# Optimization experiments

Measured on AMD Instinct MI355X. Metric: run time of the kernel, lower is better.

The kernel has to match this reference:

```python
import jax, jax.numpy as jnp
import numpy as np

D_MODEL = 512
D_STATE = 16
D_CONV = 3
EXPAND = 2
D_INNER = EXPAND * D_MODEL          # 1024
DT_RANK = -(-D_MODEL // 16)          # ceil(d_model/16) = 32
BATCH = 2
SEQ = 1024


def setup_inputs() -> dict:
    key = jax.random.key(0)
    ks = jax.random.split(key, 8)
    s = 0.02
    x = jax.random.normal(ks[0], (BATCH, SEQ, D_MODEL), jnp.float32)
    in_proj_w = jax.random.normal(ks[1], (2 * D_INNER, D_MODEL), jnp.float32) * s
    conv_w = jax.random.normal(ks[2], (D_INNER, 1, D_CONV), jnp.float32) * 0.2  # depthwise (out, in/groups=1, K)
    conv_b = jnp.zeros((D_INNER,), jnp.float32)
    x_proj_w = jax.random.normal(ks[3], (DT_RANK + 4 * D_STATE + 1, D_INNER), jnp.float32) * s
    dt_std = DT_RANK ** -0.5
    dt_w = jax.random.uniform(ks[4], (D_INNER, DT_RANK), jnp.float32, -dt_std, dt_std)
    dt = jnp.exp(jax.random.uniform(ks[5], (D_INNER,), jnp.float32)
                 * (np.log(0.1) - np.log(0.001)) + np.log(0.001))
    dt = jnp.maximum(dt, 1e-4)
    dt_b = dt + jnp.log(-jnp.expm1(-dt))  # inverse-softplus init, as in torch code
    A_log = jnp.log(jnp.tile(jnp.arange(1, D_STATE + 1, dtype=jnp.float32)[None, :], (D_INNER, 1)))
    A_imag = np.pi * jax.random.uniform(ks[6], (D_INNER, D_STATE), jnp.float32)
    D_skip = jnp.ones((D_INNER,), jnp.float32)
    out_proj_w = jax.random.normal(ks[7], (D_MODEL, D_INNER), jnp.float32) * s
    return {"x": x, "in_proj_w": in_proj_w, "conv_w": conv_w, "conv_b": conv_b,
            "x_proj_w": x_proj_w, "dt_w": dt_w, "dt_b": dt_b,
            "A_log": A_log, "A_imag": A_imag, "D_skip": D_skip,
            "out_proj_w": out_proj_w}


def _combine(c1, c2):
    # linear recurrence h_t = a_t * h_{t-1} + u_t as an associative op
    a1, u1 = c1
    a2, u2 = c2
    return a1 * a2, a2 * u1 + u2


def reference(x, in_proj_w, conv_w, conv_b, x_proj_w, dt_w, dt_b,
              A_log, A_imag, D_skip, out_proj_w):
    Bsz, L, _ = x.shape
    d_state = A_log.shape[1]
    dt_rank = dt_w.shape[1]

    xz = x @ in_proj_w.T                     # (B, L, 2*D_inner)
    xi, z = jnp.split(xz, 2, axis=-1)

    # causal depthwise conv1d (torch pads both sides K-1 then slices [:L] == left-pad K-1)
    xc = jax.lax.conv_general_dilated(
        xi.transpose(0, 2, 1), conv_w, window_strides=(1,),
        padding=[(D_CONV - 1, 0)], dimension_numbers=("NCH", "OIH", "NCH"),
        feature_group_count=conv_w.shape[0])
    xc = (xc + conv_b[None, :, None]).transpose(0, 2, 1)   # (B, L, D_inner)
    xc = jax.nn.silu(xc)

    A = -jnp.exp(A_log) + 1j * A_imag         # (D_inner, N) complex64

    proj = xc @ x_proj_w.T                     # (B, L, dt_rank + 4N + 1)
    splits = np.cumsum([dt_rank, d_state, d_state, d_state, d_state])
    delta_raw, B_re, B_im, C_re, C_im, lam = jnp.split(proj, splits, axis=-1)
    delta = jax.nn.softplus(delta_raw @ dt_w.T + dt_b)     # (B, L, D_inner)
    lam = jax.nn.sigmoid(lam)                              # (B, L, 1)
    Bc = B_re + 1j * B_im                                  # (B, L, N)
    Cc = C_re + 1j * C_im                                  # (B, L, N)

    # selective_scan_v3 (trapezoidal discretization)
    alpha = jnp.exp(delta[..., None] * A[None, None])      # (B, L, D, N) complex
    Bx = Bc[:, :, None, :] * xc[..., None]                 # (B, L, D, N) complex
    beta = (1.0 - lam)[..., None] * delta[..., None] * alpha
    gamma = lam[..., None] * delta[..., None]
    Bx_prev = jnp.pad(Bx[:, :-1], ((0, 0), (1, 0), (0, 0), (0, 0)))
    u = beta * Bx_prev + gamma * Bx                        # (B, L, D, N) complex

    _, hs = jax.lax.associative_scan(_combine, (alpha, u), axis=1)

    y = jnp.real(jnp.sum(hs * jnp.conj(Cc)[:, :, None, :], axis=-1))  # (B, L, D)
    y = y + D_skip * xc
    out = (y * jax.nn.silu(z)) @ out_proj_w.T              # (B, L, d_model)
    return out
```

## Files before the change

kernel.cpp:

```cpp
#include <hip/hip_runtime.h>

constexpr int B  = 2, L = 1024, DM = 512, DI = 1024, NST = 16, PW = 97;
constexpr int ML = B * L;
constexpr int NCHUNK = 32, CL = L / NCHUNK;
constexpr int NLANES = B * DI * NST;

#define DEV_INLINE __device__ __forceinline__

typedef __attribute__((ext_vector_type(8))) short bf16x8;
typedef __attribute__((ext_vector_type(4))) float f32x4;

DEV_INLINE float sigmoidf_(float x) { return 1.f / (1.f + __expf(-x)); }
DEV_INLINE unsigned short f2bf(float f) {
  unsigned int u = __float_as_uint(f);
  return (unsigned short)((u + 0x7FFFu + ((u >> 16) & 1u)) >> 16);
}

#if __has_builtin(__builtin_amdgcn_exp2f)
#define EXP2F(x) __builtin_amdgcn_exp2f(x)
#else
#define EXP2F(x) exp2f(x)
#endif
#if __has_builtin(__builtin_amdgcn_sinf)
#define SINR(x) __builtin_amdgcn_sinf(x)
#define COSR(x) __builtin_amdgcn_cosf(x)
#else
#define SINR(x) __sinf((x) * 6.2831853f)
#define COSR(x) __cosf((x) * 6.2831853f)
#endif

#if __has_builtin(__builtin_amdgcn_global_load_lds)
#define HAVE_GLDS 1
#define GLOAD16(g, l)                                                         \
  __builtin_amdgcn_global_load_lds(                                           \
      (const __attribute__((address_space(1))) unsigned int*)(g),             \
      (__attribute__((address_space(3))) unsigned int*)(l), 16, 0, 0)
#else
#define HAVE_GLDS 0
#endif

DEV_INLINE void sincos_poly(float th, float& s, float& c) {
  float t2 = th * th;
  float u = fmaf(t2, -1.9841270e-4f, 8.3333333e-3f);
  u = fmaf(t2, u, -0.16666667f);
  u = fmaf(t2, u, 1.f);
  s = th * u;
  float v = fmaf(t2, -1.3888889e-3f, 4.1666667e-2f);
  v = fmaf(t2, v, -0.5f);
  c = fmaf(t2, v, 1.f);
}

template <int CTRL>
DEV_INLINE float dpp_add(float v) {
  int x = __builtin_amdgcn_update_dpp(0, __float_as_int(v), CTRL, 0xF, 0xF, true);
  return v + __int_as_float(x);
}

__global__ __launch_bounds__(256) void cvt4_k(
    const float* __restrict__ i0, unsigned short* __restrict__ o0, int n0,
    const float* __restrict__ i1, unsigned short* __restrict__ o1, int n1,
    const float* __restrict__ i2, unsigned short* __restrict__ o2, int n2,
    const float* __restrict__ xw, unsigned short* __restrict__ xwpb) {
  int i = blockIdx.x * 256 + threadIdx.x;
  if (i < n0) {
    float4 v = ((const float4*)i0)[i];
    ((ushort4*)o0)[i] = make_ushort4(f2bf(v.x), f2bf(v.y), f2bf(v.z), f2bf(v.w));
  } else if (i < n0 + n1) {
    int off = i - n0;
    float4 v = ((const float4*)i1)[off];
    ((ushort4*)o1)[off] = make_ushort4(f2bf(v.x), f2bf(v.y), f2bf(v.z), f2bf(v.w));
  } else if (i < n0 + n1 + n2) {
    int off = i - n0 - n1;
    float4 v = ((const float4*)i2)[off];
    ((ushort4*)o2)[off] = make_ushort4(f2bf(v.x), f2bf(v.y), f2bf(v.z), f2bf(v.w));
  } else {
    int off = i - n0 - n1 - n2;
    if (off < 128 * 256) {
      int row = off >> 8;
      float4 v = (row < PW) ? ((const float4*)xw)[off] : make_float4(0, 0, 0, 0);
      ((ushort4*)xwpb)[off] = make_ushort4(f2bf(v.x), f2bf(v.y), f2bf(v.z), f2bf(v.w));
    }
  }
}

DEV_INLINE int swz(int row, int kb) { return (row << 7) + (kb ^ ((row & 7) << 4)); }

DEV_INLINE void stage16(const short* g, char* l) {
#if HAVE_GLDS
  GLOAD16(g, l);
#else
  *(bf16x8*)l = *(const bf16x8*)g;
#endif
}

#define GEMM_STAGE(Abase, Wbase)                                              \
  _Pragma("unroll")                                                           \
  for (int i = 0; i < 2; ++i) {                                               \
    int off = i * 4096 + tid * 16;                                            \
    int row = off >> 7, kb = off & 127;                                       \
    int kel = (kb ^ ((row & 7) << 4)) >> 1;                                   \
    stage16(Abase + (size_t)(bm + row) * K + k0 + kel, ldsb + off);           \
    stage16(Wbase + (size_t)(bn + row) * K + k0 + kel, ldsb + 8192 + off);    \
  }

#define GEMM_MFMA_BODY                                                        \
  _Pragma("unroll")                                                           \
  for (int ks = 0; ks < 2; ++ks) {                                            \
    const int kb = ks * 64 + ((lane >> 4) << 4);                              \
    bf16x8 af = *(const bf16x8*)(ldsb + swz(wv * 16 + (lane & 15), kb));      \
    _Pragma("unroll")                                                         \
    for (int nb = 0; nb < 4; ++nb) {                                          \
      bf16x8 bfv = *(const bf16x8*)(ldsb + 8192 + swz(nb * 16 + (lane & 15), kb)); \
      acc[nb] = __builtin_amdgcn_mfma_f32_16x16x32_bf16(af, bfv, acc[nb], 0, 0, 0); \
    }                                                                         \
  }

__global__ __launch_bounds__(256) void gemm_bf16_64(
    const short* __restrict__ A, const short* __restrict__ W,
    float* __restrict__ C, int M, int N, int K) {
  __shared__ char ldsb[16384];
  const int tid = threadIdx.x;
  const int lane = tid & 63, wv = tid >> 6;
  const int bm = blockIdx.y * 64, bn = blockIdx.x * 64;

  f32x4 acc[4];
#pragma unroll
  for (int nb = 0; nb < 4; ++nb) acc[nb] = (f32x4){0.f, 0.f, 0.f, 0.f};

  for (int k0 = 0; k0 < K; k0 += 64) {
    GEMM_STAGE(A, W)
    __syncthreads();
    GEMM_MFMA_BODY
    __syncthreads();
  }
#pragma unroll
  for (int nb = 0; nb < 4; ++nb) {
    int col = bn + nb * 16 + (lane & 15);
    int row0 = bm + wv * 16 + ((lane >> 4) << 2);
#pragma unroll
    for (int j = 0; j < 4; ++j)
      C[(size_t)(row0 + j) * N + col] = acc[nb][j];
  }
}

__global__ __launch_bounds__(256) void gemm_bf16_sk(
    const short* __restrict__ A, const short* __restrict__ W,
    float* __restrict__ P, int M, int N, int K, int KS) {
  __shared__ char ldsb[16384];
  const int tid = threadIdx.x;
  const int lane = tid & 63, wv = tid >> 6;
  const int bm = blockIdx.y * 64, bn = blockIdx.x * 64;
  const int kz = blockIdx.z * KS;
  float* Cp = P + (size_t)blockIdx.z * M * N;

  f32x4 acc[4];
#pragma unroll
  for (int nb = 0; nb < 4; ++nb) acc[nb] = (f32x4){0.f, 0.f, 0.f, 0.f};

  for (int k0 = kz; k0 < kz + KS; k0 += 64) {
    GEMM_STAGE(A, W)
    __syncthreads();
    GEMM_MFMA_BODY
    __syncthreads();
  }
#pragma unroll
  for (int nb = 0; nb < 4; ++nb) {
    int col = bn + nb * 16 + (lane & 15);
    int row0 = bm + wv * 16 + ((lane >> 4) << 2);
#pragma unroll
    for (int j = 0; j < 4; ++j)
      Cp[(size_t)(row0 + j) * N + col] = acc[nb][j];
  }
}

__global__ __launch_bounds__(256) void addp4_k(
    const float4* __restrict__ p, float4* __restrict__ out) {
  constexpr int NN = ML * DM / 4;
  int i = blockIdx.x * 256 + threadIdx.x;
  float4 a = p[i], b = p[i + NN], c = p[i + 2 * NN], d = p[i + 3 * NN];
  out[i] = make_float4(a.x + b.x + c.x + d.x, a.y + b.y + c.y + d.y,
                       a.z + b.z + c.z + d.z, a.w + b.w + c.w + d.w);
}

__global__ __launch_bounds__(256) void conv_silu_k(
    const float* __restrict__ xz, const float* __restrict__ cw,
    const float* __restrict__ cb, float* __restrict__ xc,
    unsigned short* __restrict__ xcb, float* __restrict__ sz) {
  int idx = blockIdx.x * 256 + threadIdx.x;
  int m = idx >> 8, d4 = (idx & 255) * 4;
  int t = m & (L - 1);
  const float* base = xz + (size_t)m * (2 * DI);
  float4 r2 = *(const float4*)(base + d4);
  float4 r1 = (t >= 1) ? *(const float4*)(base - 2 * DI + d4) : make_float4(0, 0, 0, 0);
  float4 r0 = (t >= 2) ? *(const float4*)(base - 4 * DI + d4) : make_float4(0, 0, 0, 0);
  float4 zv = *(const float4*)(base + DI + d4);
  float wv[12];
  *(float4*)(wv + 0) = *(const float4*)(cw + d4 * 3 + 0);
  *(float4*)(wv + 4) = *(const float4*)(cw + d4 * 3 + 4);
  *(float4*)(wv + 8) = *(const float4*)(cw + d4 * 3 + 8);
  float4 bv = *(const float4*)(cb + d4);
  float rin0[4] = {r0.x, r0.y, r0.z, r0.w};
  float rin1[4] = {r1.x, r1.y, r1.z, r1.w};
  float rin2[4] = {r2.x, r2.y, r2.z, r2.w};
  float bb[4] = {bv.x, bv.y, bv.z, bv.w};
  float zz[4] = {zv.x, zv.y, zv.z, zv.w};
  float xo[4], zo[4];
#pragma unroll
  for (int j = 0; j < 4; ++j) {
    float v = bb[j];
    v = fmaf(rin0[j], wv[3 * j + 0], v);
    v = fmaf(rin1[j], wv[3 * j + 1], v);
    v = fmaf(rin2[j], wv[3 * j + 2], v);
    xo[j] = v * sigmoidf_(v);
    zo[j] = zz[j] * sigmoidf_(zz[j]);
  }
  *(float4*)(xc + (size_t)idx * 4) = make_float4(xo[0], xo[1], xo[2], xo[3]);
  ((ushort4*)xcb)[idx] = make_ushort4(f2bf(xo[0]), f2bf(xo[1]), f2bf(xo[2]), f2bf(xo[3]));
  *(float4*)(sz + (size_t)idx * 4) = make_float4(zo[0], zo[1], zo[2], zo[3]);
}

__global__ __launch_bounds__(256) void reduce_delta_k(
    const float* __restrict__ P, const float* __restrict__ dtw,
    const float* __restrict__ dtb, const float* __restrict__ xc,
    float* __restrict__ bcc4, float* __restrict__ lamv,
    float2* __restrict__ dx2) {
  __shared__ float pp[2][32];
  const int tid = threadIdx.x;
  const int i = blockIdx.x * 256 + tid;
  const int m = i >> 7, c = i & 127;
  float s = 0.f;
#pragma unroll
  for (int z = 0; z < 8; ++z) s += P[(size_t)z * ML * 128 + i];
  if (c < 32)       pp[tid >> 7][c] = s;
  else if (c < 48)  bcc4[(m * 16 + c - 32) * 4 + 0] = s;
  else if (c < 64)  bcc4[(m * 16 + c - 48) * 4 + 1] = s;
  else if (c < 80)  bcc4[(m * 16 + c - 64) * 4 + 2] = s;
  else if (c < 96)  bcc4[(m * 16 + c - 80) * 4 + 3] = s;
  else if (c == 96) lamv[m] = sigmoidf_(s);
  __syncthreads();
  const int d0 = tid * 4;
  const int m0 = blockIdx.x * 2;
  float4 bb4 = *(const float4*)(dtb + d0);
  float acc[2][4];
#pragma unroll
  for (int r = 0; r < 2; ++r) {
    acc[r][0] = bb4.x; acc[r][1] = bb4.y; acc[r][2] = bb4.z; acc[r][3] = bb4.w;
  }
#pragma unroll
  for (int j = 0; j < 4; ++j) {
    const float4* wrow = (const float4*)(dtw + (size_t)(d0 + j) * 32);
#pragma unroll
    for (int kq = 0; kq < 8; ++kq) {
      float4 w4 = wrow[kq];
#pragma unroll
      for (int r = 0; r < 2; ++r) {
        acc[r][j] = fmaf(pp[r][kq * 4 + 0], w4.x, acc[r][j]);
        acc[r][j] = fmaf(pp[r][kq * 4 + 1], w4.y, acc[r][j]);
        acc[r][j] = fmaf(pp[r][kq * 4 + 2], w4.z, acc[r][j]);
        acc[r][j] = fmaf(pp[r][kq * 4 + 3], w4.w, acc[r][j]);
      }
    }
  }
#pragma unroll
  for (int r = 0; r < 2; ++r) {
    float4 xv = *(const float4*)(xc + (size_t)(m0 + r) * DI + d0);
    float dl[4];
#pragma unroll
    for (int j = 0; j < 4; ++j) {
      float xq = acc[r][j];
      dl[j] = (xq > 20.f) ? xq : log1pf(__expf(xq));
    }
    *(float4*)(dx2 + (size_t)(m0 + r) * DI + d0) = make_float4(dl[0], xv.x, dl[1], xv.y);
    *(float4*)(dx2 + (size_t)(m0 + r) * DI + d0 + 2) = make_float4(dl[2], xv.z, dl[3], xv.w);
  }
}

template <bool PASS_B>
__global__ __launch_bounds__(256, 8) void scan_pass(
    const float2* __restrict__ dx2, const float* __restrict__ lamv,
    const float4* __restrict__ bcc4, const float* __restrict__ sz,
    const float* __restrict__ A_log, const float* __restrict__ A_imag,
    const float* __restrict__ D_skip,
    float2* __restrict__ aggA, float2* __restrict__ aggU,
    unsigned short* __restrict__ ybuf) {
  __shared__ float4 qx[CL][17];
  __shared__ float2 bcl[PASS_B ? 1 : CL][17];
  __shared__ float4 bccl[PASS_B ? CL : 1][17];
  __shared__ float  ylds[PASS_B ? CL : 1][17];

  const int tid = threadIdx.x;
  const int n = tid & 15, ch = tid >> 4;
  const int bx = blockIdx.x, c = blockIdx.y;
  const int b = bx >> 6, d0 = (bx & 63) * 16;
  const int d = d0 + ch;
  const int lane = bx * 256 + tid;
  const int t0 = c * CL, mb = b * L;

  {
    int t = tid >> 3, pr = tid & 7;
    size_t row = (size_t)(mb + t0 + t);
    float4 v = *(const float4*)(dx2 + row * DI + d0 + pr * 2);
    float lamt = lamv[row];
    float g0 = lamt * v.x, g1 = lamt * v.z;
    qx[t][pr * 2 + 0] = make_float4(v.x, v.y, v.x - g0, g0);
    qx[t][pr * 2 + 1] = make_float4(v.z, v.w, v.z - g1, g1);
    float4 b0 = bcc4[row * 16 + pr * 2 + 0];
    float4 b1 = bcc4[row * 16 + pr * 2 + 1];
    if constexpr (PASS_B) {
      bccl[t][pr * 2 + 0] = b0;
      bccl[t][pr * 2 + 1] = b1;
    } else {
      bcl[t][pr * 2 + 0] = make_float2(b0.x, b0.y);
      bcl[t][pr * 2 + 1] = make_float2(b1.x, b1.y);
    }
  }

  const float Ar = -__expf(A_log[d * 16 + n]);
  const float Arl = Ar * 1.44269504f;
  const float Ai = A_imag[d * 16 + n];

  float Bxpr = 0.f, Bxpi = 0.f;
  if (c > 0) {
    float xp = dx2[(size_t)(mb + t0 - 1) * DI + d].y;
    float4 bp = bcc4[(size_t)(mb + t0 - 1) * 16 + n];
    Bxpr = bp.x * xp; Bxpi = bp.y * xp;
  }
  float hr = 0.f, hi = 0.f, S = 0.f, Dsk = 0.f;
  if (PASS_B) {
    if (c > 0) {
      float2 h0 = aggU[(c - 1) * NLANES + lane];
      hr = h0.x; hi = h0.y;
    }
    Dsk = D_skip[d];
  }

  __syncthreads();

#pragma unroll
  for (int t = 0; t < CL; ++t) {
    float4 q = qx[t][ch];
    float Br_, Bi_, Cr_ = 0.f, Ci_ = 0.f;
    if constexpr (PASS_B) {
      float4 p = bccl[t][n];
      Br_ = p.x; Bi_ = p.y; Cr_ = p.z; Ci_ = p.w;
    } else {
      float2 p = bcl[t][n];
      Br_ = p.x; Bi_ = p.y;
    }
    float ear = EXP2F(q.x * Arl);
    float sn, cs; sincos_poly(q.x * Ai, sn, cs);
    float ar = ear * cs, ai = ear * sn;
    float Bxr = Br_ * q.y, Bxi = Bi_ * q.y;
    float wr = fmaf(q.z, Bxpr, hr), wi = fmaf(q.z, Bxpi, hi);
    hr = fmaf(q.w, Bxr, fmaf(-ai, wi, ar * wr));
    hi = fmaf(q.w, Bxi, fmaf(ai, wr, ar * wi));
    Bxpr = Bxr; Bxpi = Bxi;
    if constexpr (!PASS_B) {
      S += q.x;
    } else {
      float yc = fmaf(hi, Ci_, hr * Cr_);
      yc = dpp_add<0xB1>(yc);
      yc = dpp_add<0x4E>(yc);
      yc = dpp_add<0x124>(yc);
      yc = dpp_add<0x128>(yc);
      if (n == 0) ylds[t][ch] = fmaf(Dsk, q.y, yc);
    }
  }

  if constexpr (!PASS_B) {
    float earS = EXP2F(S * Arl);
    float rvS = S * Ai * 0.15915494f;
    float AaR = earS * COSR(rvS);
    float AaI = earS * SINR(rvS);
    int idx = c * NLANES + lane;
    aggA[idx] = make_float2(AaR, AaI);
    aggU[idx] = make_float2(hr, hi);
  } else {
    __syncthreads();
    int t = tid >> 3, pr = tid & 7;
    size_t row = (size_t)(mb + t0 + t);
    float2 szv = *(const float2*)(sz + row * DI + d0 + pr * 2);
    float y0 = ylds[t][pr * 2 + 0] * szv.x;
    float y1 = ylds[t][pr * 2 + 1] * szv.y;
    unsigned pk = (unsigned)f2bf(y0) | ((unsigned)f2bf(y1) << 16);
    *(unsigned*)(ybuf + row * DI + d0 + pr * 2) = pk;
  }
}

__global__ __launch_bounds__(256) void scan_combine_k(
    const float2* __restrict__ aggA, float2* __restrict__ aggU) {
  int gid = blockIdx.x * 256 + threadIdx.x;
  float hr = 0.f, hi = 0.f;
#pragma unroll
  for (int c = 0; c < NCHUNK - 1; ++c) {
    float2 a = aggA[c * NLANES + gid];
    float2 u = aggU[c * NLANES + gid];
    float nr = fmaf(a.x, hr, fmaf(-a.y, hi, u.x));
    float ni = fmaf(a.x, hi, fmaf(a.y, hr, u.y));
    hr = nr; hi = ni;
    aggU[c * NLANES + gid] = make_float2(hr, hi);
  }
}

extern "C" void kernel_launch(void* const* d_in, const int* in_sizes, int n_in,
                              void* d_out, int out_size, void* d_ws, size_t ws_size,
                              hipStream_t stream) {
  const float* x        = (const float*)d_in[0];
  const float* in_proj  = (const float*)d_in[1];
  const float* conv_w   = (const float*)d_in[2];
  const float* conv_b   = (const float*)d_in[3];
  const float* x_proj_w = (const float*)d_in[4];
  const float* dt_w     = (const float*)d_in[5];
  const float* dt_b     = (const float*)d_in[6];
  const float* A_log    = (const float*)d_in[7];
  const float* A_imag   = (const float*)d_in[8];
  const float* D_skip   = (const float*)d_in[9];
  const float* out_proj = (const float*)d_in[10];
  float* out = (float*)d_out;

  float* ws = (float*)d_ws;
  float*  xz    = ws; ws += (size_t)ML * 2 * DI;
  float*  xc    = ws; ws += (size_t)ML * DI;
  float*  sz    = ws; ws += (size_t)ML * DI;
  float2* dx2   = (float2*)ws; ws += (size_t)ML * DI * 2;
  float*  bcc4  = ws; ws += (size_t)ML * 64;
  float*  lamv  = ws; ws += ML;
  float2* aggA  = (float2*)ws; ws += (size_t)NCHUNK * NLANES * 2;
  float2* aggU  = (float2*)ws; ws += (size_t)NCHUNK * NLANES * 2;
  unsigned short* xb   = (unsigned short*)ws; ws += (size_t)ML * DM / 2;
  unsigned short* wb1  = (unsigned short*)ws; ws += (size_t)(2 * DI) * DM / 2;
  unsigned short* wb2  = (unsigned short*)ws; ws += (size_t)DM * DI / 2;
  unsigned short* xcb  = (unsigned short*)ws; ws += (size_t)ML * DI / 2;
  unsigned short* xwpb = (unsigned short*)ws; ws += (size_t)128 * DI / 2;
  unsigned short* ybuf = (unsigned short*)ws; ws += (size_t)ML * DI / 2;

  const int n0 = ML * DM / 4, n1 = 2 * DI * DM / 4, n2 = DM * DI / 4;
  const int n3 = 128 * DI / 4;
  cvt4_k<<<(n0 + n1 + n2 + n3 + 255) / 256, 256, 0, stream>>>(
      x, xb, n0, in_proj, wb1, n1, out_proj, wb2, n2, x_proj_w, xwpb);
  gemm_bf16_64<<<dim3(2 * DI / 64, ML / 64), 256, 0, stream>>>(
      (const short*)xb, (const short*)wb1, xz, ML, 2 * DI, DM);
  conv_silu_k<<<ML * DI / 4 / 256, 256, 0, stream>>>(xz, conv_w, conv_b, xc, xcb, sz);
  gemm_bf16_sk<<<dim3(2, ML / 64, 8), 256, 0, stream>>>(
      (const short*)xcb, (const short*)xwpb, xz, ML, 128, DI, 128);
  reduce_delta_k<<<ML * 128 / 256, 256, 0, stream>>>(xz, dt_w, dt_b, xc,
                                                     bcc4, lamv, dx2);
  scan_pass<false><<<dim3(128, NCHUNK - 1), 256, 0, stream>>>(
      dx2, lamv, (const float4*)bcc4, sz, A_log, A_imag, D_skip,
      aggA, aggU, nullptr);
  scan_combine_k<<<NLANES / 256, 256, 0, stream>>>(aggA, aggU);
  scan_pass<true><<<dim3(128, NCHUNK), 256, 0, stream>>>(
      dx2, lamv, (const float4*)bcc4, sz, A_log, A_imag, D_skip,
      aggA, aggU, ybuf);
  gemm_bf16_sk<<<dim3(DM / 64, ML / 64, 4), 256, 0, stream>>>(
      (const short*)ybuf, (const short*)wb2, xz, ML, DM, DI, 256);
  addp4_k<<<ML * DM / 4 / 256, 256, 0, stream>>>((const float4*)xz, (float4*)out);
}
```

Measured before the change: 127.5 us.

## Fuse z-gate SiLU into in_proj GEMM epilogue, drop fp32 xc buffer, pack complex math

The in_proj GEMM epilogue now applies SiLU to the z half and writes it straight into the gate buffer, so conv_silu no longer reads z or writes sz. The fp32 xc buffer is removed and reduce_delta reads the bf16 copy instead, which lowers memory traffic but stores x in the scan inputs at bf16 precision. The complex recurrence math in the scan and combine kernels is rewritten with 2-wide vector helpers in the hope of getting packed FMA instructions.

Result: no change. 126.5 us (median of 2 runs) (-0.7%).

```diff
diff --git a/kernel.cpp b/kernel.cpp
--- a/kernel.cpp
+++ b/kernel.cpp
@@ -9,11 +9,25 @@
 
 typedef __attribute__((ext_vector_type(8))) short bf16x8;
 typedef __attribute__((ext_vector_type(4))) float f32x4;
+typedef __attribute__((ext_vector_type(2))) float v2f;
 
 DEV_INLINE float sigmoidf_(float x) { return 1.f / (1.f + __expf(-x)); }
 DEV_INLINE unsigned short f2bf(float f) {
   unsigned int u = __float_as_uint(f);
   return (unsigned short)((u + 0x7FFFu + ((u >> 16) & 1u)) >> 16);
+}
+DEV_INLINE float bf2f(unsigned short u) {
+  return __uint_as_float((unsigned)u << 16);
+}
+
+DEV_INLINE v2f pk_fma(float s, v2f v, v2f c) {
+  v2f r; r.x = fmaf(s, v.x, c.x); r.y = fmaf(s, v.y, c.y); return r;
+}
+DEV_INLINE v2f pk_mul(float s, v2f v) {
+  v2f r; r.x = s * v.x; r.y = s * v.y; return r;
+}
+DEV_INLINE v2f swapneg(v2f w) {
+  v2f r; r.x = -w.y; r.y = w.x; return r;
 }
 
 #if __has_builtin(__builtin_amdgcn_exp2f)
@@ -115,9 +129,9 @@
     }                                                                         \
   }
 
-__global__ __launch_bounds__(256) void gemm_bf16_64(
+__global__ __launch_bounds__(256) void gemm1_k(
     const short* __restrict__ A, const short* __restrict__ W,
-    float* __restrict__ C, int M, int N, int K) {
+    float* __restrict__ C, float* __restrict__ szp, int M, int N, int K) {
   __shared__ char ldsb[16384];
   const int tid = threadIdx.x;
   const int lane = tid & 63, wv = tid >> 6;
@@ -133,13 +147,19 @@
     GEMM_MFMA_BODY
     __syncthreads();
   }
+  const bool zside = (bn >= DI);
 #pragma unroll
   for (int nb = 0; nb < 4; ++nb) {
     int col = bn + nb * 16 + (lane & 15);
     int row0 = bm + wv * 16 + ((lane >> 4) << 2);
 #pragma unroll
-    for (int j = 0; j < 4; ++j)
-      C[(size_t)(row0 + j) * N + col] = acc[nb][j];
+    for (int j = 0; j < 4; ++j) {
+      float v = acc[nb][j];
+      if (zside)
+        szp[(size_t)(row0 + j) * DI + col - DI] = v * sigmoidf_(v);
+      else
+        C[(size_t)(row0 + j) * N + col] = v;
+    }
   }
 }
 
@@ -184,8 +204,7 @@
 
 __global__ __launch_bounds__(256) void conv_silu_k(
     const float* __restrict__ xz, const float* __restrict__ cw,
-    const float* __restrict__ cb, float* __restrict__ xc,
-    unsigned short* __restrict__ xcb, float* __restrict__ sz) {
+    const float* __restrict__ cb, unsigned short* __restrict__ xcb) {
   int idx = blockIdx.x * 256 + threadIdx.x;
   int m = idx >> 8, d4 = (idx & 255) * 4;
   int t = m & (L - 1);
@@ -193,7 +212,6 @@
   float4 r2 = *(const float4*)(base + d4);
   float4 r1 = (t >= 1) ? *(const float4*)(base - 2 * DI + d4) : make_float4(0, 0, 0, 0);
   float4 r0 = (t >= 2) ? *(const float4*)(base - 4 * DI + d4) : make_float4(0, 0, 0, 0);
-  float4 zv = *(const float4*)(base + DI + d4);
   float wv[12];
   *(float4*)(wv + 0) = *(const float4*)(cw + d4 * 3 + 0);
   *(float4*)(wv + 4) = *(const float4*)(cw + d4 * 3 + 4);
@@ -203,8 +221,7 @@
   float rin1[4] = {r1.x, r1.y, r1.z, r1.w};
   float rin2[4] = {r2.x, r2.y, r2.z, r2.w};
   float bb[4] = {bv.x, bv.y, bv.z, bv.w};
-  float zz[4] = {zv.x, zv.y, zv.z, zv.w};
-  float xo[4], zo[4];
+  float xo[4];
 #pragma unroll
   for (int j = 0; j < 4; ++j) {
     float v = bb[j];
@@ -212,16 +229,13 @@
     v = fmaf(rin1[j], wv[3 * j + 1], v);
     v = fmaf(rin2[j], wv[3 * j + 2], v);
     xo[j] = v * sigmoidf_(v);
-    zo[j] = zz[j] * sigmoidf_(zz[j]);
-  }
-  *(float4*)(xc + (size_t)idx * 4) = make_float4(xo[0], xo[1], xo[2], xo[3]);
+  }
   ((ushort4*)xcb)[idx] = make_ushort4(f2bf(xo[0]), f2bf(xo[1]), f2bf(xo[2]), f2bf(xo[3]));
-  *(float4*)(sz + (size_t)idx * 4) = make_float4(zo[0], zo[1], zo[2], zo[3]);
 }
 
 __global__ __launch_bounds__(256) void reduce_delta_k(
     const float* __restrict__ P, const float* __restrict__ dtw,
-    const float* __restrict__ dtb, const float* __restrict__ xc,
+    const float* __restrict__ dtb, const unsigned short* __restrict__ xcb,
     float* __restrict__ bcc4, float* __restrict__ lamv,
     float2* __restrict__ dx2) {
   __shared__ float pp[2][32];
@@ -263,15 +277,17 @@
   }
 #pragma unroll
   for (int r = 0; r < 2; ++r) {
-    float4 xv = *(const float4*)(xc + (size_t)(m0 + r) * DI + d0);
+    ushort4 xv = ((const ushort4*)xcb)[((size_t)(m0 + r) * DI + d0) >> 2];
     float dl[4];
 #pragma unroll
     for (int j = 0; j < 4; ++j) {
       float xq = acc[r][j];
       dl[j] = (xq > 20.f) ? xq : log1pf(__expf(xq));
     }
-    *(float4*)(dx2 + (size_t)(m0 + r) * DI + d0) = make_float4(dl[0], xv.x, dl[1], xv.y);
-    *(float4*)(dx2 + (size_t)(m0 + r) * DI + d0 + 2) = make_float4(dl[2], xv.z, dl[3], xv.w);
+    *(float4*)(dx2 + (size_t)(m0 + r) * DI + d0) =
+        make_float4(dl[0], bf2f(xv.x), dl[1], bf2f(xv.y));
+    *(float4*)(dx2 + (size_t)(m0 + r) * DI + d0 + 2) =
+        make_float4(dl[2], bf2f(xv.z), dl[3], bf2f(xv.w));
   }
 }
 
@@ -319,17 +335,18 @@
   const float Arl = Ar * 1.44269504f;
   const float Ai = A_imag[d * 16 + n];
 
-  float Bxpr = 0.f, Bxpi = 0.f;
+  v2f Bxp = (v2f){0.f, 0.f};
   if (c > 0) {
     float xp = dx2[(size_t)(mb + t0 - 1) * DI + d].y;
     float4 bp = bcc4[(size_t)(mb + t0 - 1) * 16 + n];
-    Bxpr = bp.x * xp; Bxpi = bp.y * xp;
-  }
-  float hr = 0.f, hi = 0.f, S = 0.f, Dsk = 0.f;
+    Bxp.x = bp.x * xp; Bxp.y = bp.y * xp;
+  }
+  v2f h = (v2f){0.f, 0.f};
+  float S = 0.f, Dsk = 0.f;
   if (PASS_B) {
     if (c > 0) {
       float2 h0 = aggU[(c - 1) * NLANES + lane];
-      hr = h0.x; hi = h0.y;
+      h.x = h0.x; h.y = h0.y;
     }
     Dsk = D_skip[d];
   }
@@ -339,26 +356,26 @@
 #pragma unroll
   for (int t = 0; t < CL; ++t) {
     float4 q = qx[t][ch];
-    float Br_, Bi_, Cr_ = 0.f, Ci_ = 0.f;
+    v2f Bv; float Cr_ = 0.f, Ci_ = 0.f;
     if constexpr (PASS_B) {
       float4 p = bccl[t][n];
-      Br_ = p.x; Bi_ = p.y; Cr_ = p.z; Ci_ = p.w;
+      Bv.x = p.x; Bv.y = p.y; Cr_ = p.z; Ci_ = p.w;
     } else {
       float2 p = bcl[t][n];
-      Br_ = p.x; Bi_ = p.y;
+      Bv.x = p.x; Bv.y = p.y;
     }
     float ear = EXP2F(q.x * Arl);
     float sn, cs; sincos_poly(q.x * Ai, sn, cs);
     float ar = ear * cs, ai = ear * sn;
-    float Bxr = Br_ * q.y, Bxi = Bi_ * q.y;
-    float wr = fmaf(q.z, Bxpr, hr), wi = fmaf(q.z, Bxpi, hi);
-    hr = fmaf(q.w, Bxr, fmaf(-ai, wi, ar * wr));
-    hi = fmaf(q.w, Bxi, fmaf(ai, wr, ar * wi));
-    Bxpr = Bxr; Bxpi = Bxi;
+    v2f Bx = pk_mul(q.y, Bv);
+    v2f w = pk_fma(q.z, Bxp, h);
+    v2f tg = pk_mul(q.w, Bx);
+    h = pk_fma(ar, w, pk_fma(ai, swapneg(w), tg));
+    Bxp = Bx;
     if constexpr (!PASS_B) {
       S += q.x;
     } else {
-      float yc = fmaf(hi, Ci_, hr * Cr_);
+      float yc = fmaf(h.y, Ci_, h.x * Cr_);
       yc = dpp_add<0xB1>(yc);
       yc = dpp_add<0x4E>(yc);
       yc = dpp_add<0x124>(yc);
@@ -374,7 +391,7 @@
     float AaI = earS * SINR(rvS);
     int idx = c * NLANES + lane;
     aggA[idx] = make_float2(AaR, AaI);
-    aggU[idx] = make_float2(hr, hi);
+    aggU[idx] = make_float2(h.x, h.y);
   } else {
     __syncthreads();
     int t = tid >> 3, pr = tid & 7;
@@ -390,15 +407,14 @@
 __global__ __launch_bounds__(256) void scan_combine_k(
     const float2* __restrict__ aggA, float2* __restrict__ aggU) {
   int gid = blockIdx.x * 256 + threadIdx.x;
-  float hr = 0.f, hi = 0.f;
+  v2f h = (v2f){0.f, 0.f};
 #pragma unroll
   for (int c = 0; c < NCHUNK - 1; ++c) {
     float2 a = aggA[c * NLANES + gid];
     float2 u = aggU[c * NLANES + gid];
-    float nr = fmaf(a.x, hr, fmaf(-a.y, hi, u.x));
-    float ni = fmaf(a.x, hi, fmaf(a.y, hr, u.y));
-    hr = nr; hi = ni;
-    aggU[c * NLANES + gid] = make_float2(hr, hi);
+    v2f uv; uv.x = u.x; uv.y = u.y;
+    h = pk_fma(a.x, h, pk_fma(a.y, swapneg(h), uv));
+    aggU[c * NLANES + gid] = make_float2(h.x, h.y);
   }
 }
 
@@ -420,7 +436,6 @@
 
   float* ws = (float*)d_ws;
   float*  xz    = ws; ws += (size_t)ML * 2 * DI;
-  float*  xc    = ws; ws += (size_t)ML * DI;
   float*  sz    = ws; ws += (size_t)ML * DI;
   float2* dx2   = (float2*)ws; ws += (size_t)ML * DI * 2;
   float*  bcc4  = ws; ws += (size_t)ML * 64;
@@ -438,12 +453,12 @@
   const int n3 = 128 * DI / 4;
   cvt4_k<<<(n0 + n1 + n2 + n3 + 255) / 256, 256, 0, stream>>>(
       x, xb, n0, in_proj, wb1, n1, out_proj, wb2, n2, x_proj_w, xwpb);
-  gemm_bf16_64<<<dim3(2 * DI / 64, ML / 64), 256, 0, stream>>>(
-      (const short*)xb, (const short*)wb1, xz, ML, 2 * DI, DM);
-  conv_silu_k<<<ML * DI / 4 / 256, 256, 0, stream>>>(xz, conv_w, conv_b, xc, xcb, sz);
+  gemm1_k<<<dim3(2 * DI / 64, ML / 64), 256, 0, stream>>>(
+      (const short*)xb, (const short*)wb1, xz, sz, ML, 2 * DI, DM);
+  conv_silu_k<<<ML * DI / 4 / 256, 256, 0, stream>>>(xz, conv_w, conv_b, xcb);
   gemm_bf16_sk<<<dim3(2, ML / 64, 8), 256, 0, stream>>>(
       (const short*)xcb, (const short*)xwpb, xz, ML, 128, DI, 128);
-  reduce_delta_k<<<ML * 128 / 256, 256, 0, stream>>>(xz, dt_w, dt_b, xc,
+  reduce_delta_k<<<ML * 128 / 256, 256, 0, stream>>>(xz, dt_w, dt_b, xcb,
                                                      bcc4, lamv, dx2);
   scan_pass<false><<<dim3(128, NCHUNK - 1), 256, 0, stream>>>(
       dx2, lamv, (const float4*)bcc4, sz, A_log, A_imag, D_skip,
```
